# Kernel tuning notes

Measured on AMD Instinct MI355X. Metric: run time of the kernel, lower is better.

The kernel has to match this reference:

```python
import jax, jax.numpy as jnp
import numpy as np

N_NODES = 50000
N_EDGES = 65536
D_NODE = 1024
D_HID = 1024


def setup_inputs() -> dict:
    key = jax.random.key(0)
    k1, k2, k3, k4, k5 = jax.random.split(key, 5)
    node_feats = jax.random.normal(k1, (N_NODES, D_NODE), dtype=jnp.float32)
    src = jax.random.randint(k2, (N_EDGES,), 0, N_NODES, dtype=jnp.int64)
    dst = jax.random.randint(k3, (N_EDGES,), 0, N_NODES, dtype=jnp.int64)
    # MLP([2048, 1024, 1024]) with ReLU between layers, bias, no BN, no dropout
    W1 = jax.random.normal(k4, (2 * D_NODE, D_HID), dtype=jnp.float32) * (1.0 / np.sqrt(2 * D_NODE))
    b1 = jnp.zeros((D_HID,), dtype=jnp.float32)
    W2 = jax.random.normal(k5, (D_HID, D_HID), dtype=jnp.float32) * (1.0 / np.sqrt(D_HID))
    b2 = jnp.zeros((D_HID,), dtype=jnp.float32)
    return {"node_feats": node_feats, "src": src, "dst": dst,
            "W1": W1, "b1": b1, "W2": W2, "b2": b2}


def reference(node_feats, src, dst, W1, b1, W2, b2):
    # gather per-edge src/dst node features and concat: [E, 2d]
    feat = jnp.concatenate([node_feats[src], node_feats[dst]], axis=1)
    # edge MLP: Linear -> ReLU -> Linear
    h = jax.nn.relu(feat @ W1 + b1)
    e_f = h @ W2 + b2  # [E, D_HID]
    return e_f
```

## Files before the change

kernel.cpp:

```cpp
#include <hip/hip_runtime.h>
#include <stdint.h>
#include <stddef.h>

typedef unsigned short u16;
typedef __bf16 bf16_t;
typedef bf16_t bf16x8 __attribute__((ext_vector_type(8)));
typedef float f32x4 __attribute__((ext_vector_type(4)));
typedef u16 u16x4 __attribute__((ext_vector_type(4)));

#define N_NODES 50000
#define N_EDGES 65536
#define D_NODE 1024
#define D_HID 1024

#define BM 256
#define BK 64
#define BUFE (BM * BK)
#define LDS_BYTES (4 * BUFE * 2)


__device__ __forceinline__ u16 f2bf(float f) {
  union { float f; uint32_t u; } v; v.f = f;
  uint32_t u = v.u;
  u += 0x7FFF + ((u >> 16) & 1);
  return (u16)(u >> 16);
}

typedef __attribute__((address_space(1))) const void GV;
typedef __attribute__((address_space(3))) void LV;

__device__ __forceinline__ void gll16(const void* g, void* lds_wave_base) {
  __builtin_amdgcn_global_load_lds((GV*)g, (LV*)lds_wave_base, 16, 0, 0);
}


__global__ void detect_i64_kernel(const int* __restrict__ src, int* __restrict__ flag) {
  if (threadIdx.x == 0 && blockIdx.x == 0) {
    int o = 0;
    for (int i = 1; i < 32; i += 2) o |= src[i];
    *flag = (o == 0) ? 1 : 0;
  }
}

__global__ void cvt_bf16_kernel(const float* __restrict__ in, u16* __restrict__ out, size_t n4) {
  size_t i = (size_t)blockIdx.x * blockDim.x + threadIdx.x;
  if (i >= n4) return;
  float4 v = reinterpret_cast<const float4*>(in)[i];
  u16x4 o;
  o.x = f2bf(v.x); o.y = f2bf(v.y); o.z = f2bf(v.z); o.w = f2bf(v.w);
  reinterpret_cast<u16x4*>(out)[i] = o;
}

__global__ void transpose_cvt_kernel(const float* __restrict__ in, u16* __restrict__ out,
                                     int K, int N) {
  __shared__ float tile[32][33];
  int n0 = blockIdx.x * 32, k0 = blockIdx.y * 32;
  int tx = threadIdx.x, ty = threadIdx.y;
  #pragma unroll
  for (int i = ty; i < 32; i += 8)
    tile[i][tx] = in[(size_t)(k0 + i) * N + (n0 + tx)];
  __syncthreads();
  #pragma unroll
  for (int i = ty; i < 32; i += 8)
    out[(size_t)(n0 + i) * K + (k0 + tx)] = f2bf(tile[tx][i]);
}


template <bool FIRST>
__device__ __forceinline__ void gemm_body(const u16* __restrict__ Abf,
                                          const int* __restrict__ src,
                                          const int* __restrict__ dst,
                                          const int* __restrict__ is64p,
                                          const u16* __restrict__ Bt,
                                          const float* __restrict__ bias,
                                          u16* __restrict__ hout,
                                          float* __restrict__ fout,
                                          const int K) {
  extern __shared__ __align__(16) u16 lds[];
  u16* const ldsA = lds;
  u16* const ldsB = lds + 2 * BUFE;

  const int t = threadIdx.x;
  const int lane = t & 63;
  const int wave = t >> 6;

  const int b = blockIdx.x;
  const int wgid = (b & 7) * 128 + (b >> 3);
  const int bm = (wgid >> 2) * BM;
  const int bn = (wgid & 3) * BM;

  const int wm = (wave >> 2) * 128;
  const int wn = (wave & 3) * 64;

  const int srow = t >> 3;
  const int kswz = (((t & 7) ^ (srow & 7)) << 3);
  const int stoff = wave * 512;

  const u16* ap[4];
  const u16* ad[4];
  const u16* bp[4];
  if constexpr (FIRST) {
    const int is64 = *is64p;
    #pragma unroll
    for (int q = 0; q < 4; ++q) {
      const int e = bm + q * 64 + srow;
      const int s = is64 ? src[2 * e] : src[e];
      const int d = is64 ? dst[2 * e] : dst[e];
      ap[q] = Abf + (size_t)s * D_NODE + kswz;
      ad[q] = Abf + (size_t)d * D_NODE + kswz;
    }
  } else {
    #pragma unroll
    for (int q = 0; q < 4; ++q) {
      ap[q] = Abf + (size_t)(bm + q * 64 + srow) * K + kswz;
      ad[q] = nullptr;
    }
  }
  #pragma unroll
  for (int q = 0; q < 4; ++q)
    bp[q] = Bt + (size_t)(bn + q * 64 + srow) * K + kswz;

  auto stageA = [&](int buf, int q, int u) {
    const u16* g;
    if constexpr (FIRST) {
      g = (u < (D_NODE / BK)) ? (ap[q] + u * BK) : (ad[q] + (u - D_NODE / BK) * BK);
    } else {
      g = ap[q] + u * BK;
    }
    gll16(g, ldsA + buf * BUFE + q * 4096 + stoff);
  };
  auto stageB = [&](int buf, int q, int u) {
    gll16(bp[q] + u * BK, ldsB + buf * BUFE + q * 4096 + stoff);
  };

  const int lm = lane & 15;
  const int kq8 = ((lane >> 4) & 3) << 3;
  const int swzr = (lm & 7) << 3;
  const int kb0 = kq8 ^ swzr;
  const int kb1 = (32 + kq8) ^ swzr;
  const int arow = (wm + lm) * BK;
  const int brow = (wn + lm) * BK;

  f32x4 acc[8][4] = {};

  const int NT = K / BK;

  #pragma unroll
  for (int q = 0; q < 4; ++q) stageA(0, q, 0);
  #pragma unroll
  for (int q = 0; q < 4; ++q) stageB(0, q, 0);
  asm volatile("s_waitcnt vmcnt(0)" ::: "memory");
  __builtin_amdgcn_s_barrier();

  for (int u = 0; u < NT; ++u) {
    const int cb = u & 1;
    const u16* As_c = ldsA + cb * BUFE;
    const u16* Bs_c = ldsB + cb * BUFE;

    if (u + 1 < NT) {
      const int nb = cb ^ 1;
      stageA(nb, 0, u + 1); stageA(nb, 1, u + 1);
      stageA(nb, 2, u + 1); stageA(nb, 3, u + 1);
      stageB(nb, 0, u + 1); stageB(nb, 1, u + 1);
      stageB(nb, 2, u + 1); stageB(nb, 3, u + 1);
    }

    bf16x8 aq[4], ar[4], bq[4], br[4];

    #pragma unroll
    for (int j = 0; j < 4; ++j)
      bq[j] = *reinterpret_cast<const bf16x8*>(Bs_c + brow + j * 1024 + kb0);
    #pragma unroll
    for (int i = 0; i < 4; ++i)
      aq[i] = *reinterpret_cast<const bf16x8*>(As_c + arow + i * 1024 + kb0);
    #pragma unroll
    for (int i = 0; i < 4; ++i)
      ar[i] = *reinterpret_cast<const bf16x8*>(As_c + arow + (i + 4) * 1024 + kb0);

    __builtin_amdgcn_s_setprio(1);
    #pragma unroll
    for (int i = 0; i < 4; ++i)
      #pragma unroll
      for (int j = 0; j < 4; ++j)
        acc[i][j] = __builtin_amdgcn_mfma_f32_16x16x32_bf16(aq[i], bq[j], acc[i][j], 0, 0, 0);
    __builtin_amdgcn_s_setprio(0);

    #pragma unroll
    for (int j = 0; j < 4; ++j)
      br[j] = *reinterpret_cast<const bf16x8*>(Bs_c + brow + j * 1024 + kb1);
    #pragma unroll
    for (int i = 0; i < 4; ++i)
      aq[i] = *reinterpret_cast<const bf16x8*>(As_c + arow + i * 1024 + kb1);

    __builtin_amdgcn_s_setprio(1);
    #pragma unroll
    for (int i = 0; i < 4; ++i)
      #pragma unroll
      for (int j = 0; j < 4; ++j)
        acc[i + 4][j] = __builtin_amdgcn_mfma_f32_16x16x32_bf16(ar[i], bq[j], acc[i + 4][j], 0, 0, 0);
    __builtin_amdgcn_s_setprio(0);

    #pragma unroll
    for (int i = 0; i < 4; ++i)
      ar[i] = *reinterpret_cast<const bf16x8*>(As_c + arow + (i + 4) * 1024 + kb1);

    __builtin_amdgcn_s_setprio(1);
    #pragma unroll
    for (int i = 0; i < 4; ++i)
      #pragma unroll
      for (int j = 0; j < 4; ++j)
        acc[i][j] = __builtin_amdgcn_mfma_f32_16x16x32_bf16(aq[i], br[j], acc[i][j], 0, 0, 0);
    #pragma unroll
    for (int i = 0; i < 4; ++i)
      #pragma unroll
      for (int j = 0; j < 4; ++j)
        acc[i + 4][j] = __builtin_amdgcn_mfma_f32_16x16x32_bf16(ar[i], br[j], acc[i + 4][j], 0, 0, 0);
    __builtin_amdgcn_s_setprio(0);

    asm volatile("s_waitcnt vmcnt(0)" ::: "memory");
    __builtin_amdgcn_s_barrier();
  }

  const int rq = ((lane >> 4) & 3) * 4;
  #pragma unroll
  for (int j = 0; j < 4; ++j) {
    const int n = bn + wn + 16 * j + lm;
    const float bj = bias[n];
    #pragma unroll
    for (int i = 0; i < 8; ++i) {
      const int m0 = bm + wm + 16 * i + rq;
      f32x4 c = acc[i][j];
      #pragma unroll
      for (int rr = 0; rr < 4; ++rr) {
        float vv = c[rr] + bj;
        if (FIRST) {
          vv = fmaxf(vv, 0.0f);
          hout[(size_t)(m0 + rr) * D_HID + n] = f2bf(vv);
        } else {
          fout[(size_t)(m0 + rr) * D_HID + n] = vv;
        }
      }
    }
  }
}

__launch_bounds__(512, 2)
__global__ void gemm1_kernel(const u16* __restrict__ Abf, const int* __restrict__ src,
                             const int* __restrict__ dst, const int* __restrict__ is64p,
                             const u16* __restrict__ Bt, const float* __restrict__ bias,
                             u16* __restrict__ hout) {
  gemm_body<true>(Abf, src, dst, is64p, Bt, bias, hout, nullptr, 2 * D_NODE);
}

__launch_bounds__(512, 2)
__global__ void gemm2_kernel(const u16* __restrict__ Abf, const u16* __restrict__ Bt,
                             const float* __restrict__ bias, float* __restrict__ fout) {
  gemm_body<false>(Abf, nullptr, nullptr, nullptr, Bt, bias, nullptr, fout, D_HID);
}


extern "C" void kernel_launch(void* const* d_in, const int* in_sizes, int n_in,
                              void* d_out, int out_size, void* d_ws, size_t ws_size,
                              hipStream_t stream) {
  const float* node_feats = (const float*)d_in[0];
  const int*   src        = (const int*)d_in[1];
  const int*   dst        = (const int*)d_in[2];
  const float* W1         = (const float*)d_in[3];
  const float* b1         = (const float*)d_in[4];
  const float* W2         = (const float*)d_in[5];
  const float* b2         = (const float*)d_in[6];
  float* out = (float*)d_out;

  u16* ws = (u16*)d_ws;
  const size_t NODE_E = (size_t)N_NODES * D_NODE;
  u16* node_bf = ws;
  u16* W1T = node_bf + NODE_E;
  u16* W2T = W1T + (size_t)2048 * 1024;
  u16* h   = W2T + (size_t)1024 * 1024;
  int* flag = (int*)(h + (size_t)N_EDGES * D_HID);

  static bool attr_set = false;
  if (!attr_set) {
    hipFuncSetAttribute(reinterpret_cast<const void*>(&gemm1_kernel),
                        hipFuncAttributeMaxDynamicSharedMemorySize, LDS_BYTES);
    hipFuncSetAttribute(reinterpret_cast<const void*>(&gemm2_kernel),
                        hipFuncAttributeMaxDynamicSharedMemorySize, LDS_BYTES);
    attr_set = true;
  }

  detect_i64_kernel<<<1, 64, 0, stream>>>(src, flag);

  cvt_bf16_kernel<<<(unsigned)(NODE_E / 4 / 256), 256, 0, stream>>>(node_feats, node_bf, NODE_E / 4);

  transpose_cvt_kernel<<<dim3(1024 / 32, 2048 / 32), dim3(32, 8), 0, stream>>>(W1, W1T, 2048, 1024);
  transpose_cvt_kernel<<<dim3(1024 / 32, 1024 / 32), dim3(32, 8), 0, stream>>>(W2, W2T, 1024, 1024);

  gemm1_kernel<<<1024, 512, LDS_BYTES, stream>>>(node_bf, src, dst, flag, W1T, b1, h);

  gemm2_kernel<<<1024, 512, LDS_BYTES, stream>>>(h, W2T, b2, out);
}
```

Measured before the change: 804.8 us.

## Deepen GEMM load pipeline to two tiles ahead with mid-iteration LDS reuse barrier

The prologue now stages two k-tiles, and each iteration issues the global-to-LDS loads for tile u+2 into the buffer currently being consumed. It does this only after all LDS fragment reads for that buffer have finished, enforced with an lgkmcnt wait and a mid-iteration barrier. The end-of-iteration wait becomes vmcnt(8) so one tile's loads stay in flight, hiding more global latency. This costs an extra barrier per iteration and more live fragment registers (aq2/ar2), which may raise register pressure.

Result: no change. 804.5 us (-0.0%).

```diff
diff --git a/kernel.cpp b/kernel.cpp
--- a/kernel.cpp
+++ b/kernel.cpp
@@ -132,6 +132,10 @@
   auto stageB = [&](int buf, int q, int u) {
     gll16(bp[q] + u * BK, ldsB + buf * BUFE + q * 4096 + stoff);
   };
+  auto stageGroup = [&](int buf, int u) {
+    stageA(buf, 0, u); stageA(buf, 1, u); stageA(buf, 2, u); stageA(buf, 3, u);
+    stageB(buf, 0, u); stageB(buf, 1, u); stageB(buf, 2, u); stageB(buf, 3, u);
+  };
 
   const int lm = lane & 15;
   const int kq8 = ((lane >> 4) & 3) << 3;
@@ -145,11 +149,9 @@
 
   const int NT = K / BK;
 
-  #pragma unroll
-  for (int q = 0; q < 4; ++q) stageA(0, q, 0);
-  #pragma unroll
-  for (int q = 0; q < 4; ++q) stageB(0, q, 0);
-  asm volatile("s_waitcnt vmcnt(0)" ::: "memory");
+  stageGroup(0, 0);
+  stageGroup(1, 1);
+  asm volatile("s_waitcnt vmcnt(8)" ::: "memory");
   __builtin_amdgcn_s_barrier();
 
   for (int u = 0; u < NT; ++u) {
@@ -157,14 +159,6 @@
     const u16* As_c = ldsA + cb * BUFE;
     const u16* Bs_c = ldsB + cb * BUFE;
 
-    if (u + 1 < NT) {
-      const int nb = cb ^ 1;
-      stageA(nb, 0, u + 1); stageA(nb, 1, u + 1);
-      stageA(nb, 2, u + 1); stageA(nb, 3, u + 1);
-      stageB(nb, 0, u + 1); stageB(nb, 1, u + 1);
-      stageB(nb, 2, u + 1); stageB(nb, 3, u + 1);
-    }
-
     bf16x8 aq[4], ar[4], bq[4], br[4];
 
     #pragma unroll
@@ -188,9 +182,14 @@
     #pragma unroll
     for (int j = 0; j < 4; ++j)
       br[j] = *reinterpret_cast<const bf16x8*>(Bs_c + brow + j * 1024 + kb1);
-    #pragma unroll
-    for (int i = 0; i < 4; ++i)
-      aq[i] = *reinterpret_cast<const bf16x8*>(As_c + arow + i * 1024 + kb1);
+    bf16x8 aq2[4];
+    #pragma unroll
+    for (int i = 0; i < 4; ++i)
+      aq2[i] = *reinterpret_cast<const bf16x8*>(As_c + arow + i * 1024 + kb1);
+    bf16x8 ar2[4];
+    #pragma unroll
+    for (int i = 0; i < 4; ++i)
+      ar2[i] = *reinterpret_cast<const bf16x8*>(As_c + arow + (i + 4) * 1024 + kb1);
 
     __builtin_amdgcn_s_setprio(1);
     #pragma unroll
@@ -200,24 +199,28 @@
         acc[i + 4][j] = __builtin_amdgcn_mfma_f32_16x16x32_bf16(ar[i], bq[j], acc[i + 4][j], 0, 0, 0);
     __builtin_amdgcn_s_setprio(0);
 
-    #pragma unroll
-    for (int i = 0; i < 4; ++i)
-      ar[i] = *reinterpret_cast<const bf16x8*>(As_c + arow + (i + 4) * 1024 + kb1);
+    asm volatile("s_waitcnt lgkmcnt(0)" ::: "memory");
+    __builtin_amdgcn_sched_barrier(0);
+    __builtin_amdgcn_s_barrier();
+    __builtin_amdgcn_sched_barrier(0);
+
+    if (u + 2 < NT) stageGroup(cb, u + 2);
 
     __builtin_amdgcn_s_setprio(1);
     #pragma unroll
     for (int i = 0; i < 4; ++i)
       #pragma unroll
       for (int j = 0; j < 4; ++j)
-        acc[i][j] = __builtin_amdgcn_mfma_f32_16x16x32_bf16(aq[i], br[j], acc[i][j], 0, 0, 0);
+        acc[i][j] = __builtin_amdgcn_mfma_f32_16x16x32_bf16(aq2[i], br[j], acc[i][j], 0, 0, 0);
     #pragma unroll
     for (int i = 0; i < 4; ++i)
       #pragma unroll
       for (int j = 0; j < 4; ++j)
-        acc[i + 4][j] = __builtin_amdgcn_mfma_f32_16x16x32_bf16(ar[i], br[j], acc[i + 4][j], 0, 0, 0);
+        acc[i + 4][j] = __builtin_amdgcn_mfma_f32_16x16x32_bf16(ar2[i], br[j], acc[i + 4][j], 0, 0, 0);
     __builtin_amdgcn_s_setprio(0);
 
-    asm volatile("s_waitcnt vmcnt(0)" ::: "memory");
+    if (u + 2 < NT)      asm volatile("s_waitcnt vmcnt(8)" ::: "memory");
+    else if (u + 1 < NT) asm volatile("s_waitcnt vmcnt(0)" ::: "memory");
     __builtin_amdgcn_s_barrier();
   }
 
```
